# Kernel tuning notes

Hardware: AMD Instinct MI355X
Metric: run time of the kernel (lower is better)

Reference implementation:

```python
import jax, jax.numpy as jnp
import numpy as np

NUM_EMBEDDINGS = 512
EMBEDDING_DIM = 128

def setup_inputs() -> dict:
    key = jax.random.key(0)
    k1, k2 = jax.random.split(key)
    z_e = jax.random.normal(k1, (32, EMBEDDING_DIM, 64, 64), dtype=jnp.float32)
    embedding = jax.random.normal(k2, (NUM_EMBEDDINGS, EMBEDDING_DIM), dtype=jnp.float32)
    return {"z_e": z_e, "embedding": embedding}

def reference(z_e, embedding):
    B, C, H, W = z_e.shape
    # (B,C,H,W) -> (N, C) with N = B*H*W
    z_flat = jnp.transpose(z_e, (0, 2, 3, 1)).reshape(-1, C)
    # squared L2 distance via expansion: ||z||^2 - 2 z.E^T + ||E||^2  (avoids (N,K,C) intermediate)
    z_sq = jnp.sum(z_flat * z_flat, axis=-1, keepdims=True)          # (N,1)
    e_sq = jnp.sum(embedding * embedding, axis=-1)                    # (K,)
    dist = z_sq - 2.0 * jnp.einsum('nc,kc->nk', z_flat, embedding) + e_sq  # (N,K)
    indices = jnp.argmin(dist, axis=1)                                # (N,)
    z_q = embedding[indices].reshape(B, H, W, C)                      # gather
    return jnp.transpose(z_q, (0, 3, 1, 2))                           # (B,C,H,W)
```

## Files before the change

kernel.cpp:

```cpp
#include <hip/hip_runtime.h>
#include <float.h>

#define NUM_EMB 512
#define DIM     128
#define HWX     4096
#define NPOS    (32 * 4096)
#define MARGIN  0.35f
#define EPS1    0.175f

#define WS_WL    ((size_t)0)
#define WS_E16   ((size_t)524288)
#define WS_ESQ   ((size_t)655360)
#define WS_CNT   ((size_t)657408)
#define WS_NEED  ((size_t)657664)

using half8 = __attribute__((ext_vector_type(8))) _Float16;
using f32x4 = __attribute__((ext_vector_type(4))) float;

__global__ void prep_kernel(const float* __restrict__ emb, _Float16* __restrict__ e16,
                            float* __restrict__ esq, int* __restrict__ cnt) {
    int k = blockIdx.x * blockDim.x + threadIdx.x;
    if (k == 0) { cnt[0] = 0; cnt[1] = 0; }
    if (k < NUM_EMB) {
        const float4* row = (const float4*)(emb + (size_t)k * DIM);
        _Float16* dst = e16 + (size_t)k * DIM;
        float s0 = 0.f, s1 = 0.f, s2 = 0.f, s3 = 0.f;
        #pragma unroll
        for (int c = 0; c < DIM / 4; ++c) {
            float4 v = row[c];
            s0 = fmaf(v.x, v.x, s0);
            s1 = fmaf(v.y, v.y, s1);
            s2 = fmaf(v.z, v.z, s2);
            s3 = fmaf(v.w, v.w, s3);
            dst[4 * c + 0] = (_Float16)v.x;
            dst[4 * c + 1] = (_Float16)v.y;
            dst[4 * c + 2] = (_Float16)v.z;
            dst[4 * c + 3] = (_Float16)v.w;
        }
        esq[k] = (s0 + s1) + (s2 + s3);
    }
}

__global__ __launch_bounds__(256) void gemm_argmin(const float* __restrict__ z,
                                                   const _Float16* __restrict__ e16,
                                                   const float* __restrict__ esq,
                                                   const float* __restrict__ emb,
                                                   float* __restrict__ out,
                                                   int* __restrict__ wl,
                                                   int* __restrict__ cnt) {
    __shared__ __align__(16) char Ash[128 * 272];
    __shared__ float mB1[2][128];
    __shared__ float mB2[2][128];
    __shared__ float mB3[2][128];
    __shared__ float msh[128];
    __shared__ int   ish[128];

    int t = threadIdx.x;
    int lane = t & 63, wave = t >> 6;
    int wm = wave & 1, wn = wave >> 1;
    int quad = lane >> 4, l15 = lane & 15;
    int n0 = blockIdx.x * 128;
    int bb = n0 >> 12;
    int hw0 = n0 & 4095;

    {
        int g = t & 31, cq = t >> 5;
        int hw = hw0 + 4 * g;
        const float* zp = z + (size_t)bb * DIM * HWX + (size_t)cq * 16 * HWX + hw;
        char* arow0 = Ash + (4 * g) * 272;
        int xr = g & 7;
        #pragma unroll
        for (int k = 0; k < 2; ++k) {
            float4 v[8];
            #pragma unroll
            for (int c = 0; c < 8; ++c)
                v[c] = *(const float4*)(zp + (size_t)(k * 8 + c) * HWX);
            int slotb = ((2 * cq + k) ^ xr) * 16;
            #pragma unroll
            for (int j = 0; j < 4; ++j) {
                half8 hv;
                #pragma unroll
                for (int c = 0; c < 8; ++c) {
                    float f = (j == 0) ? v[c].x : (j == 1) ? v[c].y
                            : (j == 2) ? v[c].z : v[c].w;
                    hv[c] = (_Float16)f;
                }
                *(half8*)(arow0 + j * 272 + slotb) = hv;
            }
        }
    }
    __syncthreads();

    float b1[16], b2[16], b3[16];
    #pragma unroll
    for (int s = 0; s < 16; ++s) { b1[s] = 3.0e38f; b2[s] = 3.0e38f; b3[s] = 3.0e38f; }

    const char* abase = Ash + (wm * 64 + l15) * 272 + (quad ^ (l15 >> 2)) * 16;
    const char* ebase = (const char*)e16 + ((size_t)(wn * 32 + l15) << 8) + quad * 16;
    const float* eqb  = esq + wn * 32 + l15;

    for (int tile = 0; tile < 8; ++tile) {
        half8 bf[2][4];
        {
            const char* eb = ebase + (size_t)tile * 64 * 256;
            #pragma unroll
            for (int nt = 0; nt < 2; ++nt)
                #pragma unroll
                for (int kc = 0; kc < 4; ++kc)
                    bf[nt][kc] = *(const half8*)(eb + nt * 4096 + kc * 64);
        }
        float es0 = eqb[tile * 64];
        float es1 = eqb[tile * 64 + 16];

        f32x4 acc[4][2];
        #pragma unroll
        for (int mt = 0; mt < 4; ++mt)
            #pragma unroll
            for (int nt = 0; nt < 2; ++nt)
                acc[mt][nt] = (f32x4){0.f, 0.f, 0.f, 0.f};

        #pragma unroll
        for (int kc = 0; kc < 4; ++kc) {
            half8 af[4];
            #pragma unroll
            for (int mt = 0; mt < 4; ++mt)
                af[mt] = *(const half8*)(abase + mt * (16 * 272) + ((kc ^ (mt & 1)) * 64));
            #pragma unroll
            for (int mt = 0; mt < 4; ++mt)
                #pragma unroll
                for (int nt = 0; nt < 2; ++nt)
                    acc[mt][nt] = __builtin_amdgcn_mfma_f32_16x16x32_f16(af[mt], bf[nt][kc], acc[mt][nt], 0, 0, 0);
        }

        #pragma unroll
        for (int nt = 0; nt < 2; ++nt) {
            unsigned code = (unsigned)(tile * 64 + wn * 32 + nt * 16 + l15);
            float es = nt ? es1 : es0;
            #pragma unroll
            for (int mt = 0; mt < 4; ++mt)
                #pragma unroll
                for (int r = 0; r < 4; ++r) {
                    int s = mt * 4 + r;
                    float sc = fmaf(-2.0f, acc[mt][nt][r], es);
                    float p = __uint_as_float((__float_as_uint(sc) & 0xFFFFFE00u) | code);
                    float t1 = fmaxf(b1[s], p);
                    b1[s] = fminf(b1[s], p);
                    float t2 = fmaxf(b2[s], t1);
                    b2[s] = fminf(b2[s], t1);
                    b3[s] = fminf(b3[s], t2);
                }
        }
    }

    #pragma unroll
    for (int d = 1; d < 16; d <<= 1) {
        #pragma unroll
        for (int s = 0; s < 16; ++s) {
            float o1 = __shfl_xor(b1[s], d, 64);
            float o2 = __shfl_xor(b2[s], d, 64);
            float o3 = __shfl_xor(b3[s], d, 64);
            float u1 = fmaxf(b1[s], o1);
            b1[s] = fminf(b1[s], o1);
            float l2 = fminf(b2[s], o2);
            float w  = fmaxf(u1, l2);
            b2[s] = fminf(u1, l2);
            b3[s] = fminf(fminf(b3[s], o3), w);
        }
    }
    if (l15 == 0) {
        #pragma unroll
        for (int s = 0; s < 16; ++s) {
            int m = wm * 64 + (s >> 2) * 16 + quad * 4 + (s & 3);
            mB1[wn][m] = b1[s];
            mB2[wn][m] = b2[s];
            mB3[wn][m] = b3[s];
        }
    }
    __syncthreads();
    if (t < 128) {
        float a1 = mB1[0][t], c1 = mB1[1][t];
        float a2 = mB2[0][t], c2 = mB2[1][t];
        float a3 = mB3[0][t], c3 = mB3[1][t];
        float u1 = fmaxf(a1, c1);
        float m1 = fminf(a1, c1);
        float l2 = fminf(a2, c2);
        float m2 = fminf(u1, l2);
        float m3 = fminf(fminf(a3, c3), fmaxf(u1, l2));
        int ix1 = (int)(__float_as_uint(m1) & 511u);
        int ix2 = (int)(__float_as_uint(m2) & 511u);
        ish[t] = ix1 | (ix2 << 9);
        msh[t] = m3;
    }
    __syncthreads();

    {
        int g = t & 31, cq = t >> 5;
        int hw = hw0 + 4 * g;
        const float* zp = z + (size_t)bb * DIM * HWX + (size_t)cq * 16 * HWX + hw;
        int ii[4];
        #pragma unroll
        for (int j = 0; j < 4; ++j) ii[j] = ish[4 * g + j];
        float d1[4] = {0.f, 0.f, 0.f, 0.f};
        float d2[4] = {0.f, 0.f, 0.f, 0.f};
        #pragma unroll
        for (int k = 0; k < 2; ++k) {
            float4 v[8];
            #pragma unroll
            for (int c = 0; c < 8; ++c)
                v[c] = *(const float4*)(zp + (size_t)(k * 8 + c) * HWX);
            #pragma unroll
            for (int j = 0; j < 4; ++j) {
                const float* e1p = emb + (size_t)(ii[j] & 511) * DIM + cq * 16 + k * 8;
                const float* e2p = emb + (size_t)((ii[j] >> 9) & 511) * DIM + cq * 16 + k * 8;
                float4 p0 = *(const float4*)(e1p), p1 = *(const float4*)(e1p + 4);
                float4 q0 = *(const float4*)(e2p), q1 = *(const float4*)(e2p + 4);
                float e1c[8] = {p0.x, p0.y, p0.z, p0.w, p1.x, p1.y, p1.z, p1.w};
                float e2c[8] = {q0.x, q0.y, q0.z, q0.w, q1.x, q1.y, q1.z, q1.w};
                #pragma unroll
                for (int c = 0; c < 8; ++c) {
                    float zc = (j == 0) ? v[c].x : (j == 1) ? v[c].y
                             : (j == 2) ? v[c].z : v[c].w;
                    d1[j] = fmaf(zc, e1c[c], d1[j]);
                    d2[j] = fmaf(zc, e2c[c], d2[j]);
                }
            }
        }
        float2* part = (float2*)Ash;
        #pragma unroll
        for (int j = 0; j < 4; ++j)
            part[(4 * g + j) * 9 + cq] = make_float2(d1[j], d2[j]);
    }
    __syncthreads();
    if (t < 128) {
        int ii = ish[t];
        int i1 = ii & 511, i2 = (ii >> 9) & 511;
        const float2* pr = (const float2*)Ash + (size_t)t * 9;
        float d1 = 0.f, d2 = 0.f;
        #pragma unroll
        for (int cq = 0; cq < 8; ++cq) {
            float2 pv = pr[cq];
            d1 += pv.x;
            d2 += pv.y;
        }
        float s1 = fmaf(-2.f, d1, esq[i1]);
        float s2 = fmaf(-2.f, d2, esq[i2]);
        bool take2 = (s2 < s1) || (s2 == s1 && i2 < i1);
        ish[t] = take2 ? i2 : i1;
        if (fminf(s1, s2) >= msh[t] - EPS1) {
            int p = atomicAdd(cnt, 1);
            wl[p] = n0 + t;
        }
    }
    __syncthreads();

    {
        int g = t & 31, cq = t >> 5;
        int hw = hw0 + 4 * g;
        int i0 = ish[4 * g + 0], i1v = ish[4 * g + 1];
        int i2 = ish[4 * g + 2], i3 = ish[4 * g + 3];
        const float4* e0 = (const float4*)(emb + (size_t)i0 * DIM) + cq * 4;
        const float4* e1 = (const float4*)(emb + (size_t)i1v * DIM) + cq * 4;
        const float4* e2 = (const float4*)(emb + (size_t)i2 * DIM) + cq * 4;
        const float4* e3 = (const float4*)(emb + (size_t)i3 * DIM) + cq * 4;
        float* ob = out + (size_t)bb * DIM * HWX + (size_t)cq * 16 * HWX + hw;
        #pragma unroll
        for (int cc = 0; cc < 4; ++cc) {
            float4 r0 = e0[cc], r1 = e1[cc], r2 = e2[cc], r3 = e3[cc];
            *(float4*)(ob + (size_t)(4 * cc + 0) * HWX) = (float4){r0.x, r1.x, r2.x, r3.x};
            *(float4*)(ob + (size_t)(4 * cc + 1) * HWX) = (float4){r0.y, r1.y, r2.y, r3.y};
            *(float4*)(ob + (size_t)(4 * cc + 2) * HWX) = (float4){r0.z, r1.z, r2.z, r3.z};
            *(float4*)(ob + (size_t)(4 * cc + 3) * HWX) = (float4){r0.w, r1.w, r2.w, r3.w};
        }
    }
}

__global__ __launch_bounds__(256) void refine_kernel(const float* __restrict__ z,
                                                     const float* __restrict__ emb,
                                                     const float* __restrict__ esq,
                                                     const int* __restrict__ wl,
                                                     const int* __restrict__ cnt,
                                                     float* __restrict__ out) {
    __shared__ __align__(16) float zsh[16][132];
    __shared__ int nsh[16];
    __shared__ int ksh[16];

    int t = threadIdx.x, lane = t & 63, wave = t >> 6;
    int count = *cnt;

    for (int base = blockIdx.x * 16; base < count; base += gridDim.x * 16) {
        {
            int e = t >> 4, d = t & 15;
            int ge = base + e;
            if (ge > count - 1) ge = count - 1;
            int n = wl[ge];
            if (d == 0) nsh[e] = n;
            int b = n >> 12, hw = n & 4095;
            const float* zp = z + (size_t)b * DIM * HWX + hw;
            #pragma unroll
            for (int jj = 0; jj < 8; ++jj)
                zsh[e][d + 16 * jj] = zp[(size_t)(d + 16 * jj) * HWX];
        }
        __syncthreads();

        int e0 = wave * 4;
        float acc[4][8];
        #pragma unroll
        for (int e = 0; e < 4; ++e)
            #pragma unroll
            for (int j = 0; j < 8; ++j) acc[e][j] = 0.f;

        const float* ebase = emb + (size_t)lane * DIM;
        #pragma unroll 4
        for (int c4 = 0; c4 < 32; ++c4) {
            float4 zv[4];
            #pragma unroll
            for (int e = 0; e < 4; ++e)
                zv[e] = *(const float4*)&zsh[e0 + e][c4 * 4];
            float4 ev[8];
            #pragma unroll
            for (int j = 0; j < 8; ++j)
                ev[j] = *(const float4*)(ebase + (size_t)j * 64 * DIM + c4 * 4);
            #pragma unroll
            for (int e = 0; e < 4; ++e)
                #pragma unroll
                for (int j = 0; j < 8; ++j) {
                    acc[e][j] = fmaf(zv[e].x, ev[j].x, acc[e][j]);
                    acc[e][j] = fmaf(zv[e].y, ev[j].y, acc[e][j]);
                    acc[e][j] = fmaf(zv[e].z, ev[j].z, acc[e][j]);
                    acc[e][j] = fmaf(zv[e].w, ev[j].w, acc[e][j]);
                }
        }

        float esv[8];
        #pragma unroll
        for (int j = 0; j < 8; ++j) esv[j] = esq[64 * j + lane];

        float bs[4]; int bk[4];
        #pragma unroll
        for (int e = 0; e < 4; ++e) {
            bs[e] = 3.0e38f; bk[e] = 0;
            #pragma unroll
            for (int j = 0; j < 8; ++j) {
                float s = fmaf(-2.f, acc[e][j], esv[j]);
                if (s < bs[e]) { bs[e] = s; bk[e] = 64 * j + lane; }
            }
        }
        #pragma unroll
        for (int d = 1; d < 64; d <<= 1) {
            #pragma unroll
            for (int e = 0; e < 4; ++e) {
                float os = __shfl_xor(bs[e], d, 64);
                int   ok = __shfl_xor(bk[e], d, 64);
                bool take = (os < bs[e]) || (os == bs[e] && ok < bk[e]);
                bs[e] = take ? os : bs[e];
                bk[e] = take ? ok : bk[e];
            }
        }
        if (lane == 0) {
            #pragma unroll
            for (int e = 0; e < 4; ++e) ksh[e0 + e] = bk[e];
        }
        __syncthreads();
        {
            int e = t >> 4, d = t & 15;
            int n = nsh[e];
            int b = n >> 12, hw = n & 4095;
            int kk = ksh[e];
            const float* er = emb + (size_t)kk * DIM;
            float* ob = out + (size_t)b * DIM * HWX + hw;
            #pragma unroll
            for (int jj = 0; jj < 8; ++jj)
                ob[(size_t)(d + 16 * jj) * HWX] = er[d + 16 * jj];
        }
        __syncthreads();
    }
}

__global__ void esq_kernel(const float* __restrict__ emb, float* __restrict__ e_sq) {
    int k = blockIdx.x * blockDim.x + threadIdx.x;
    if (k < NUM_EMB) {
        const float4* row = (const float4*)(emb + k * DIM);
        float s0 = 0.f, s1 = 0.f, s2 = 0.f, s3 = 0.f;
        #pragma unroll
        for (int c = 0; c < DIM / 4; ++c) {
            float4 v = row[c];
            s0 = fmaf(v.x, v.x, s0); s1 = fmaf(v.y, v.y, s1);
            s2 = fmaf(v.z, v.z, s2); s3 = fmaf(v.w, v.w, s3);
        }
        e_sq[k] = (s0 + s1) + (s2 + s3);
    }
}

__global__ __launch_bounds__(256) void vq_kernel(const float* __restrict__ z,
                                                 const float* __restrict__ emb,
                                                 const float* __restrict__ e_sq,
                                                 float* __restrict__ out) {
    int n = blockIdx.x * 256 + threadIdx.x;
    int b = n >> 12, hw = n & 4095;
    const float* zb = z + (size_t)b * DIM * HWX + hw;
    float zr[DIM];
    #pragma unroll
    for (int c = 0; c < DIM; ++c) zr[c] = zb[(size_t)c * HWX];
    float best = FLT_MAX; int besti = 0;
    for (int k = 0; k < NUM_EMB; ++k) {
        const float4* er = (const float4*)(emb + k * DIM);
        float d0 = 0.f, d1 = 0.f, d2 = 0.f, d3 = 0.f;
        #pragma unroll
        for (int c = 0; c < DIM / 4; ++c) {
            float4 e = er[c];
            d0 = fmaf(zr[4 * c + 0], e.x, d0);
            d1 = fmaf(zr[4 * c + 1], e.y, d1);
            d2 = fmaf(zr[4 * c + 2], e.z, d2);
            d3 = fmaf(zr[4 * c + 3], e.w, d3);
        }
        float s = e_sq[k] - 2.f * ((d0 + d1) + (d2 + d3));
        if (s < best) { best = s; besti = k; }
    }
    float* ob = out + (size_t)b * DIM * HWX + hw;
    const float4* sel = (const float4*)(emb + (size_t)besti * DIM);
    #pragma unroll
    for (int c4 = 0; c4 < DIM / 4; ++c4) {
        float4 v = sel[c4];
        ob[(size_t)(4 * c4 + 0) * HWX] = v.x;
        ob[(size_t)(4 * c4 + 1) * HWX] = v.y;
        ob[(size_t)(4 * c4 + 2) * HWX] = v.z;
        ob[(size_t)(4 * c4 + 3) * HWX] = v.w;
    }
}

extern "C" void kernel_launch(void* const* d_in, const int* in_sizes, int n_in,
                              void* d_out, int out_size, void* d_ws, size_t ws_size,
                              hipStream_t stream) {
    const float* z   = (const float*)d_in[0];
    const float* emb = (const float*)d_in[1];
    float* out = (float*)d_out;

    if (ws_size < WS_NEED) {
        float* e_sq = (float*)d_ws;
        esq_kernel<<<(NUM_EMB + 255) / 256, 256, 0, stream>>>(emb, e_sq);
        vq_kernel<<<NPOS / 256, 256, 0, stream>>>(z, emb, e_sq, out);
        return;
    }

    char* ws = (char*)d_ws;
    _Float16* e16 = (_Float16*)(ws + WS_E16);
    float*    esq = (float*)(ws + WS_ESQ);
    int*      wl  = (int*)(ws + WS_WL);
    int*      cnt = (int*)(ws + WS_CNT);

    prep_kernel<<<2, 256, 0, stream>>>(emb, e16, esq, cnt);
    gemm_argmin<<<NPOS / 128, 256, 0, stream>>>(z, e16, esq, emb, out, wl, cnt);
    refine_kernel<<<1024, 256, 0, stream>>>(z, emb, esq, wl, cnt, out);
}
```

Measured before the change: 210.6 us.

## Fuse fp32 refinement of ambiguous positions into the GEMM argmin kernel

```diff
diff --git a/kernel.cpp b/kernel.cpp
--- a/kernel.cpp
+++ b/kernel.cpp
@@ -5,22 +5,18 @@
 #define DIM     128
 #define HWX     4096
 #define NPOS    (32 * 4096)
-#define MARGIN  0.35f
 #define EPS1    0.175f
 
-#define WS_WL    ((size_t)0)
-#define WS_E16   ((size_t)524288)
-#define WS_ESQ   ((size_t)655360)
-#define WS_CNT   ((size_t)657408)
-#define WS_NEED  ((size_t)657664)
+#define WS_E16   ((size_t)0)
+#define WS_ESQ   ((size_t)131072)
+#define WS_NEED  ((size_t)133120)
 
 using half8 = __attribute__((ext_vector_type(8))) _Float16;
 using f32x4 = __attribute__((ext_vector_type(4))) float;
 
 __global__ void prep_kernel(const float* __restrict__ emb, _Float16* __restrict__ e16,
-                            float* __restrict__ esq, int* __restrict__ cnt) {
+                            float* __restrict__ esq) {
     int k = blockIdx.x * blockDim.x + threadIdx.x;
-    if (k == 0) { cnt[0] = 0; cnt[1] = 0; }
     if (k < NUM_EMB) {
         const float4* row = (const float4*)(emb + (size_t)k * DIM);
         _Float16* dst = e16 + (size_t)k * DIM;
@@ -45,15 +41,14 @@
                                                    const _Float16* __restrict__ e16,
                                                    const float* __restrict__ esq,
                                                    const float* __restrict__ emb,
-                                                   float* __restrict__ out,
-                                                   int* __restrict__ wl,
-                                                   int* __restrict__ cnt) {
+                                                   float* __restrict__ out) {
     __shared__ __align__(16) char Ash[128 * 272];
     __shared__ float mB1[2][128];
     __shared__ float mB2[2][128];
     __shared__ float mB3[2][128];
     __shared__ float msh[128];
     __shared__ int   ish[128];
+    __shared__ int   bcnt;
 
     int t = threadIdx.x;
     int lane = t & 63, wave = t >> 6;
@@ -62,6 +57,8 @@
     int n0 = blockIdx.x * 128;
     int bb = n0 >> 12;
     int hw0 = n0 & 4095;
+
+    if (t == 0) bcnt = 0;
 
     {
         int g = t & 31, cq = t >> 5;
@@ -247,11 +244,66 @@
         bool take2 = (s2 < s1) || (s2 == s1 && i2 < i1);
         ish[t] = take2 ? i2 : i1;
         if (fminf(s1, s2) >= msh[t] - EPS1) {
-            int p = atomicAdd(cnt, 1);
-            wl[p] = n0 + t;
+            int q = atomicAdd(&bcnt, 1);
+            ((int*)&mB1[1][0])[q] = t;
         }
     }
     __syncthreads();
+
+    {
+        int nf = bcnt;
+        float* zrow = &mB1[0][0];
+        const int* fl = (const int*)&mB1[1][0];
+        for (int f = 0; f < nf; ++f) {
+            int p = fl[f];
+            if (t < 128)
+                zrow[t] = z[(size_t)bb * DIM * HWX + (size_t)t * HWX + (hw0 + p)];
+            __syncthreads();
+            int k1 = t, k2 = t + 256;
+            const float* ea = emb + (size_t)k1 * DIM;
+            const float* eb = emb + (size_t)k2 * DIM;
+            float da = 0.f, db = 0.f;
+            #pragma unroll 8
+            for (int c4 = 0; c4 < 32; ++c4) {
+                float4 zv = *(const float4*)&zrow[c4 * 4];
+                float4 va = *(const float4*)(ea + c4 * 4);
+                float4 vb = *(const float4*)(eb + c4 * 4);
+                da = fmaf(zv.x, va.x, da); da = fmaf(zv.y, va.y, da);
+                da = fmaf(zv.z, va.z, da); da = fmaf(zv.w, va.w, da);
+                db = fmaf(zv.x, vb.x, db); db = fmaf(zv.y, vb.y, db);
+                db = fmaf(zv.z, vb.z, db); db = fmaf(zv.w, vb.w, db);
+            }
+            float sa = fmaf(-2.f, da, esq[k1]);
+            float sb = fmaf(-2.f, db, esq[k2]);
+            float bs = sa; int bk = k1;
+            if (sb < bs) { bs = sb; bk = k2; }
+            #pragma unroll
+            for (int d = 1; d < 64; d <<= 1) {
+                float os = __shfl_xor(bs, d, 64);
+                int   ok = __shfl_xor(bk, d, 64);
+                bool take = (os < bs) || (os == bs && ok < bk);
+                bs = take ? os : bs;
+                bk = take ? ok : bk;
+            }
+            if (lane == 0) {
+                mB2[0][wave] = bs;
+                ((int*)&mB2[1][0])[wave] = bk;
+            }
+            __syncthreads();
+            if (t == 0) {
+                float s = mB2[0][0]; int k = ((int*)&mB2[1][0])[0];
+                #pragma unroll
+                for (int w = 1; w < 4; ++w) {
+                    float s2 = mB2[0][w]; int k2b = ((int*)&mB2[1][0])[w];
+                    bool take = (s2 < s) || (s2 == s && k2b < k);
+                    s = take ? s2 : s;
+                    k = take ? k2b : k;
+                }
+                ish[p] = k;
+            }
+            __syncthreads();
+        }
+    }
 
     {
         int g = t & 31, cq = t >> 5;
@@ -271,108 +323,6 @@
             *(float4*)(ob + (size_t)(4 * cc + 2) * HWX) = (float4){r0.z, r1.z, r2.z, r3.z};
             *(float4*)(ob + (size_t)(4 * cc + 3) * HWX) = (float4){r0.w, r1.w, r2.w, r3.w};
         }
-    }
-}
-
-__global__ __launch_bounds__(256) void refine_kernel(const float* __restrict__ z,
-                                                     const float* __restrict__ emb,
-                                                     const float* __restrict__ esq,
-                                                     const int* __restrict__ wl,
-                                                     const int* __restrict__ cnt,
-                                                     float* __restrict__ out) {
-    __shared__ __align__(16) float zsh[16][132];
-    __shared__ int nsh[16];
-    __shared__ int ksh[16];
-
-    int t = threadIdx.x, lane = t & 63, wave = t >> 6;
-    int count = *cnt;
-
-    for (int base = blockIdx.x * 16; base < count; base += gridDim.x * 16) {
-        {
-            int e = t >> 4, d = t & 15;
-            int ge = base + e;
-            if (ge > count - 1) ge = count - 1;
-            int n = wl[ge];
-            if (d == 0) nsh[e] = n;
-            int b = n >> 12, hw = n & 4095;
-            const float* zp = z + (size_t)b * DIM * HWX + hw;
-            #pragma unroll
-            for (int jj = 0; jj < 8; ++jj)
-                zsh[e][d + 16 * jj] = zp[(size_t)(d + 16 * jj) * HWX];
-        }
-        __syncthreads();
-
-        int e0 = wave * 4;
-        float acc[4][8];
-        #pragma unroll
-        for (int e = 0; e < 4; ++e)
-            #pragma unroll
-            for (int j = 0; j < 8; ++j) acc[e][j] = 0.f;
-
-        const float* ebase = emb + (size_t)lane * DIM;
-        #pragma unroll 4
-        for (int c4 = 0; c4 < 32; ++c4) {
-            float4 zv[4];
-            #pragma unroll
-            for (int e = 0; e < 4; ++e)
-                zv[e] = *(const float4*)&zsh[e0 + e][c4 * 4];
-            float4 ev[8];
-            #pragma unroll
-            for (int j = 0; j < 8; ++j)
-                ev[j] = *(const float4*)(ebase + (size_t)j * 64 * DIM + c4 * 4);
-            #pragma unroll
-            for (int e = 0; e < 4; ++e)
-                #pragma unroll
-                for (int j = 0; j < 8; ++j) {
-                    acc[e][j] = fmaf(zv[e].x, ev[j].x, acc[e][j]);
-                    acc[e][j] = fmaf(zv[e].y, ev[j].y, acc[e][j]);
-                    acc[e][j] = fmaf(zv[e].z, ev[j].z, acc[e][j]);
-                    acc[e][j] = fmaf(zv[e].w, ev[j].w, acc[e][j]);
-                }
-        }
-
-        float esv[8];
-        #pragma unroll
-        for (int j = 0; j < 8; ++j) esv[j] = esq[64 * j + lane];
-
-        float bs[4]; int bk[4];
-        #pragma unroll
-        for (int e = 0; e < 4; ++e) {
-            bs[e] = 3.0e38f; bk[e] = 0;
-            #pragma unroll
-            for (int j = 0; j < 8; ++j) {
-                float s = fmaf(-2.f, acc[e][j], esv[j]);
-                if (s < bs[e]) { bs[e] = s; bk[e] = 64 * j + lane; }
-            }
-        }
-        #pragma unroll
-        for (int d = 1; d < 64; d <<= 1) {
-            #pragma unroll
-            for (int e = 0; e < 4; ++e) {
-                float os = __shfl_xor(bs[e], d, 64);
-                int   ok = __shfl_xor(bk[e], d, 64);
-                bool take = (os < bs[e]) || (os == bs[e] && ok < bk[e]);
-                bs[e] = take ? os : bs[e];
-                bk[e] = take ? ok : bk[e];
-            }
-        }
-        if (lane == 0) {
-            #pragma unroll
-            for (int e = 0; e < 4; ++e) ksh[e0 + e] = bk[e];
-        }
-        __syncthreads();
-        {
-            int e = t >> 4, d = t & 15;
-            int n = nsh[e];
-            int b = n >> 12, hw = n & 4095;
-            int kk = ksh[e];
-            const float* er = emb + (size_t)kk * DIM;
-            float* ob = out + (size_t)b * DIM * HWX + hw;
-            #pragma unroll
-            for (int jj = 0; jj < 8; ++jj)
-                ob[(size_t)(d + 16 * jj) * HWX] = er[d + 16 * jj];
-        }
-        __syncthreads();
     }
 }
 
@@ -445,10 +395,7 @@
     char* ws = (char*)d_ws;
     _Float16* e16 = (_Float16*)(ws + WS_E16);
     float*    esq = (float*)(ws + WS_ESQ);
-    int*      wl  = (int*)(ws + WS_WL);
-    int*      cnt = (int*)(ws + WS_CNT);
-
-    prep_kernel<<<2, 256, 0, stream>>>(emb, e16, esq, cnt);
-    gemm_argmin<<<NPOS / 128, 256, 0, stream>>>(z, e16, esq, emb, out, wl, cnt);
-    refine_kernel<<<1024, 256, 0, stream>>>(z, emb, esq, wl, cnt, out);
+
+    prep_kernel<<<2, 256, 0, stream>>>(emb, e16, esq);
+    gemm_argmin<<<NPOS / 128, 256, 0, stream>>>(z, e16, esq, emb, out);
 }
```

New measurement: 187.5 us. -11.0%, faster.
